# Optimization experiments

Measured on AMD Instinct MI355X. Metric: run time of the kernel, lower is better.

Reference implementation:

```python
import jax, jax.numpy as jnp
import numpy as np

LEAKY_SLOPE = 0.05        # self.alpha is overwritten to 0.05 in __init__
NEG_INF = -9.0e15         # masking constant from the source
THRESH = 0.5              # connection_threshold

B, N, F = 8, 2048, 128


def setup_inputs() -> dict:
    key = jax.random.key(0)
    k1, k2, k3, k4, k5 = jax.random.split(key, 5)
    h = jax.random.normal(k1, (B, N, F), dtype=jnp.float32)
    W = jax.random.normal(k2, (F, F), dtype=jnp.float32) * (1.414 / np.sqrt(F))
    a = jax.random.normal(k3, (2 * F, 1), dtype=jnp.float32) * 0.1
    A1 = jax.random.normal(k4, (4 * N, N), dtype=jnp.float32) * (1.414 / np.sqrt(N))
    A2 = jax.random.normal(k5, (N, 4 * N), dtype=jnp.float32) * (1.414 / np.sqrt(4 * N))
    return {"h": h, "W": W, "a": a, "A1": A1, "A2": A2}


def reference(h, W, a, A1, A2):
    f = W.shape[0]
    # Wh = h @ W^T  (torch Linear stores weight as [out, in])
    Wh = jnp.einsum('bnf,gf->bng', h, W)                       # [B,N,F]
    # additive GAT scores: e[b,i,j] = leaky_relu(Wh_i.a1 + Wh_j.a2)
    Wh1 = Wh @ a[:f, :]                                        # [B,N,1]
    Wh2 = Wh @ a[f:, :]                                        # [B,N,1]
    e = Wh1 + jnp.swapaxes(Wh2, 1, 2)                          # [B,N,N]
    e = jnp.where(e > 0, e, LEAKY_SLOPE * e)                   # LeakyReLU(0.05)
    # learned adjacency gate over last dim (computed in the original forward
    # but never used for the returned output -> dead code; kept for fidelity)
    hid = jax.nn.sigmoid(jnp.einsum('bij,hj->bih', e, A1))     # [B,N,4N]
    adj = jax.nn.sigmoid(e + jnp.einsum('bih,jh->bij', hid, A2))
    adj = jnp.where(adj > THRESH, adj, 0.0)                    # unused downstream
    # masked softmax attention over e itself
    attention = jax.nn.softmax(jnp.where(e > 0, e, NEG_INF), axis=2)
    # dropout is identity in eval mode (training=False)
    h_prime = jnp.einsum('bij,bjf->bif', attention, Wh)        # [B,N,F]
    return jax.nn.elu(h_prime)                                 # concat=True branch
```

## Files before the change

### kernel.cpp

```cpp
#include <hip/hip_runtime.h>
#include <math.h>

#define BB 8
#define NN 2048
#define FF 128
#define CH 128
#define CHSZ 16

__global__ __launch_bounds__(512) void k1_wh(
        const float* __restrict__ h, const float* __restrict__ W,
        const float* __restrict__ a, float* __restrict__ Wh,
        float* __restrict__ s1, float* __restrict__ s2) {
    __shared__ __align__(16) float Wt[64][132];
    __shared__ float hs[64][65];
    const int tid = threadIdx.x;
    const int row0 = blockIdx.x * 64;
    const int gq = tid & 15;
    const int rq = tid >> 4;

    float acc[2][8];
#pragma unroll
    for (int r = 0; r < 2; ++r)
#pragma unroll
        for (int g = 0; g < 8; ++g) acc[r][g] = 0.f;

    for (int half = 0; half < 2; ++half) {
        __syncthreads();
        for (int idx = tid; idx < 64 * 128; idx += 512) {
            int g = idx >> 6, fl = idx & 63;
            Wt[fl][g] = W[g * 128 + half * 64 + fl];
        }
        for (int idx = tid; idx < 64 * 64; idx += 512) {
            int r = idx >> 6, fl = idx & 63;
            hs[r][fl] = h[(row0 + r) * 128 + half * 64 + fl];
        }
        __syncthreads();
        for (int fl = 0; fl < 64; ++fl) {
            float4 w0 = *(const float4*)&Wt[fl][gq * 8];
            float4 w1 = *(const float4*)&Wt[fl][gq * 8 + 4];
            float h0 = hs[rq * 2 + 0][fl];
            float h1 = hs[rq * 2 + 1][fl];
            acc[0][0] += h0 * w0.x; acc[0][1] += h0 * w0.y;
            acc[0][2] += h0 * w0.z; acc[0][3] += h0 * w0.w;
            acc[0][4] += h0 * w1.x; acc[0][5] += h0 * w1.y;
            acc[0][6] += h0 * w1.z; acc[0][7] += h0 * w1.w;
            acc[1][0] += h1 * w0.x; acc[1][1] += h1 * w0.y;
            acc[1][2] += h1 * w0.z; acc[1][3] += h1 * w0.w;
            acc[1][4] += h1 * w1.x; acc[1][5] += h1 * w1.y;
            acc[1][6] += h1 * w1.z; acc[1][7] += h1 * w1.w;
        }
    }

    float a1v[8], a2v[8];
#pragma unroll
    for (int g = 0; g < 8; ++g) {
        a1v[g] = a[gq * 8 + g];
        a2v[g] = a[128 + gq * 8 + g];
    }
#pragma unroll
    for (int r = 0; r < 2; ++r) {
        int row = row0 + rq * 2 + r;
        *(float4*)&Wh[row * 128 + gq * 8] =
            make_float4(acc[r][0], acc[r][1], acc[r][2], acc[r][3]);
        *(float4*)&Wh[row * 128 + gq * 8 + 4] =
            make_float4(acc[r][4], acc[r][5], acc[r][6], acc[r][7]);
        float p1 = 0.f, p2 = 0.f;
#pragma unroll
        for (int g = 0; g < 8; ++g) {
            p1 += acc[r][g] * a1v[g];
            p2 += acc[r][g] * a2v[g];
        }
#pragma unroll
        for (int s = 1; s < 16; s <<= 1) {
            p1 += __shfl_xor(p1, s, 64);
            p2 += __shfl_xor(p2, s, 64);
        }
        if (gq == 0) { s1[row] = p1; s2[row] = p2; }
    }
}

__global__ __launch_bounds__(256) void k2_rank(
        const float* __restrict__ s2, const float* __restrict__ s1,
        int* __restrict__ idxs, float* __restrict__ ps,
        int* __restrict__ lo_arr) {
    __shared__ __align__(16) float ls[NN];
    __shared__ int part[4][64];
    __shared__ int lpart[4][64];
    __shared__ float wmax[4];
    const int t = threadIdx.x;
    const int blk = blockIdx.x;
    const int b = blk >> 5;
    const int seg = blk & 31;
    const int base = b * NN;
    float4* ls4 = (float4*)ls;
    const float4* g4 = (const float4*)(s2 + base);
    float m = -INFINITY;
    for (int i = t; i < NN / 4; i += 256) {
        float4 v4 = g4[i];
        ls4[i] = v4;
        m = fmaxf(m, fmaxf(fmaxf(v4.x, v4.y), fmaxf(v4.z, v4.w)));
    }
#pragma unroll
    for (int s = 1; s < 64; s <<= 1) m = fmaxf(m, __shfl_xor(m, s, 64));
    if ((t & 63) == 0) wmax[t >> 6] = m;
    __syncthreads();
    const float M = fmaxf(fmaxf(wmax[0], wmax[1]), fmaxf(wmax[2], wmax[3]));
    const int jj = t & 63;
    const int w  = t >> 6;
    const int j  = seg * 64 + jj;
    const float v = ls[j];
    const float s1v = s1[base + j];
    int rank = 0, cnt = 0;
#pragma unroll 8
    for (int q = 0; q < 128; ++q) {
        float4 kv = ls4[w * 128 + q];
        int kg = w * 512 + q * 4;
        rank += (kv.x < v) | ((kv.x == v) & (kg + 0 < j));
        rank += (kv.y < v) | ((kv.y == v) & (kg + 1 < j));
        rank += (kv.z < v) | ((kv.z == v) & (kg + 2 < j));
        rank += (kv.w < v) | ((kv.w == v) & (kg + 3 < j));
        cnt += (s1v + kv.x <= 0.f);
        cnt += (s1v + kv.y <= 0.f);
        cnt += (s1v + kv.z <= 0.f);
        cnt += (s1v + kv.w <= 0.f);
    }
    part[w][jj] = rank;
    lpart[w][jj] = cnt;
    __syncthreads();
    if (t < 64) {
        int r = part[0][t] + part[1][t] + part[2][t] + part[3][t];
        int jg = seg * 64 + t;
        float vv = ls[jg];
        idxs[base + r] = jg;
        ps[base + r] = expf(vv - M);
        lo_arr[base + jg] = lpart[0][t] + lpart[1][t] + lpart[2][t] + lpart[3][t];
    }
}

__global__ __launch_bounds__(128) void k3_scan(
        const float* __restrict__ Wh, const int* __restrict__ idxs,
        const float* __restrict__ ps,
        float* __restrict__ partial, float* __restrict__ psuf,
        float* __restrict__ chunktot, float* __restrict__ chunku,
        float* __restrict__ chunkp) {
    const int blk = blockIdx.x;
    const int b = blk >> 7, c = blk & 127;
    const int base = b * NN;
    const int f = threadIdx.x;
    float acc = 0.f, accu = 0.f, pacc = 0.f;
#pragma unroll
    for (int tt = CHSZ - 1; tt >= 0; --tt) {
        int r = c * CHSZ + tt;
        int jj = idxs[base + r];
        float pv = ps[base + r];
        float w = Wh[(base + jj) * 128 + f];
        acc += pv * w;
        accu += w;
        pacc += pv;
        partial[(base + r) * 128 + f] = acc;
        if (f == 0) psuf[base + r] = pacc;
    }
    chunktot[(b * CH + c) * 128 + f] = acc;
    chunku[(b * CH + c) * 128 + f] = accu;
    if (f == 0) chunkp[b * CH + c] = pacc;
}

__global__ __launch_bounds__(128) void k3b_chunksuf(
        const float* __restrict__ chunktot, const float* __restrict__ chunku,
        const float* __restrict__ chunkp,
        float* __restrict__ chunksuf, float* __restrict__ chunkpsuf,
        float* __restrict__ meanv) {
    __shared__ float lt[CH][128];
    __shared__ float lp[CH];
    const int b = blockIdx.x;
    const int f = threadIdx.x;
    float tu = 0.f;
#pragma unroll 4
    for (int c = 0; c < CH; ++c) {
        lt[c][f] = chunktot[(b * CH + c) * 128 + f];
        tu += chunku[(b * CH + c) * 128 + f];
    }
    lp[f] = chunkp[b * CH + f];
    __syncthreads();
#pragma unroll
    for (int s = 1; s < CH; s <<= 1) {
        float add = (f + s < CH) ? lp[f + s] : 0.f;
        __syncthreads();
        lp[f] += add;
        __syncthreads();
    }
    chunkpsuf[b * CH + f] = (f < CH - 1) ? lp[f + 1] : 0.f;
    float acc = 0.f;
#pragma unroll 4
    for (int c = CH - 1; c >= 0; --c) {
        chunksuf[(b * CH + c) * 128 + f] = acc;
        acc += lt[c][f];
    }
    meanv[b * 128 + f] = tu * (1.f / (float)NN);
}

__global__ __launch_bounds__(256) void k4_out(
        const int* __restrict__ lo_arr, const float* __restrict__ psuf,
        const float* __restrict__ chunkpsuf, const float* __restrict__ partial,
        const float* __restrict__ chunksuf, const float* __restrict__ meanv,
        float* __restrict__ out) {
    const int tid = threadIdx.x;
    const int rowg = blockIdx.x * 8 + (tid >> 5);
    const int fq = (tid & 31) * 4;
    const int b = rowg >> 11;
    const int base = b * NN;
    const int lo = lo_arr[rowg];
    float4 v;
    if (lo == NN) {
        v = *(const float4*)&meanv[b * 128 + fq];
    } else {
        const int c = lo >> 4;
        float4 pp = *(const float4*)&partial[(base + lo) * 128 + fq];
        float4 cs = *(const float4*)&chunksuf[(b * CH + c) * 128 + fq];
        float den = psuf[base + lo] + chunkpsuf[b * CH + c];
        v.x = (pp.x + cs.x) / den;
        v.y = (pp.y + cs.y) / den;
        v.z = (pp.z + cs.z) / den;
        v.w = (pp.w + cs.w) / den;
    }
    v.x = (v.x > 0.f) ? v.x : expm1f(v.x);
    v.y = (v.y > 0.f) ? v.y : expm1f(v.y);
    v.z = (v.z > 0.f) ? v.z : expm1f(v.z);
    v.w = (v.w > 0.f) ? v.w : expm1f(v.w);
    *(float4*)&out[rowg * 128 + fq] = v;
}

extern "C" void kernel_launch(void* const* d_in, const int* in_sizes, int n_in,
                              void* d_out, int out_size, void* d_ws, size_t ws_size,
                              hipStream_t stream) {
    (void)in_sizes; (void)n_in; (void)out_size; (void)ws_size;
    const float* h = (const float*)d_in[0];
    const float* W = (const float*)d_in[1];
    const float* a = (const float*)d_in[2];
    float* out = (float*)d_out;

    float* Wh       = (float*)d_ws;
    float* partial  = Wh + 2097152;
    float* s1       = partial + 2097152;
    float* s2       = s1 + 16384;
    float* ps       = s2 + 16384;
    float* psuf     = ps + 16384;
    int*   idxs     = (int*)(psuf + 16384);
    int*   lo_arr   = idxs + 16384;
    float* chunktot = (float*)(lo_arr + 16384);
    float* chunku   = chunktot + 131072;
    float* chunksuf = chunku + 131072;
    float* chunkp   = chunksuf + 131072;
    float* chunkpsuf= chunkp + 1024;
    float* meanv    = chunkpsuf + 1024;

    k1_wh<<<BB * NN / 64, 512, 0, stream>>>(h, W, a, Wh, s1, s2);
    k2_rank<<<BB * 32, 256, 0, stream>>>(s2, s1, idxs, ps, lo_arr);
    k3_scan<<<BB * CH, 128, 0, stream>>>(Wh, idxs, ps, partial, psuf,
                                         chunktot, chunku, chunkp);
    k3b_chunksuf<<<BB, 128, 0, stream>>>(chunktot, chunku, chunkp,
                                         chunksuf, chunkpsuf, meanv);
    k4_out<<<BB * NN / 8, 256, 0, stream>>>(lo_arr, psuf, chunkpsuf,
                                            partial, chunksuf, meanv, out);
}
```

Before: 195.2 us.

## Fuse all five stages into one cooperative persistent kernel with grid syncs

Merges the Wh projection, ranking, chunk scan, chunk suffix and output stages into a single cooperative kernel of 256 blocks. Grid-wide syncs replace the kernel launch boundaries, and a shared-memory union is reused across the phases. The aim is to remove four launch gaps and their tail effects, since each stage is short. In exchange, several stages change their block decomposition (for example the k3b suffix now uses 256 blocks instead of 8). The grid syncs carry their own cost, and the old multi-kernel path is kept as a fallback for when a cooperative launch is unsupported or fails.

```diff
diff --git a/kernel.cpp b/kernel.cpp
--- a/kernel.cpp
+++ b/kernel.cpp
@@ -1,11 +1,264 @@
 #include <hip/hip_runtime.h>
+#include <hip/hip_cooperative_groups.h>
 #include <math.h>
+
+namespace cg = cooperative_groups;
 
 #define BB 8
 #define NN 2048
 #define FF 128
 #define CH 128
 #define CHSZ 16
+
+
+struct Params {
+    const float* __restrict__ h;
+    const float* __restrict__ W;
+    const float* __restrict__ a;
+    float* __restrict__ Wh;
+    float* __restrict__ partial;
+    float* __restrict__ s1;
+    float* __restrict__ s2;
+    float* __restrict__ ps;
+    float* __restrict__ psuf;
+    int*   __restrict__ idxs;
+    int*   __restrict__ lo_arr;
+    float* __restrict__ chunktot;
+    float* __restrict__ chunku;
+    float* __restrict__ chunksuf;
+    float* __restrict__ chunkp;
+    float* __restrict__ chunkpsuf;
+    float* __restrict__ meanv;
+    float* __restrict__ out;
+};
+
+union __align__(16) SMem {
+    struct { float Wt[64][132]; float hs[64][65]; } p1;
+    struct { float ls[NN]; int part[8][64]; int lpart[8][64]; float wmax[8]; } p2;
+    struct { float lt[4][132]; float lu[4][132]; float lp[CH]; } p3b;
+};
+
+__global__ __launch_bounds__(512) void fused(Params P) {
+    __shared__ SMem sm;
+    const int tid = threadIdx.x;
+    const int blk = blockIdx.x;
+    cg::grid_group grid = cg::this_grid();
+
+    {
+        const int row0 = blk * 64;
+        const int gq = tid & 15;
+        const int rq = tid >> 4;
+
+        float acc[2][8];
+#pragma unroll
+        for (int r = 0; r < 2; ++r)
+#pragma unroll
+            for (int g = 0; g < 8; ++g) acc[r][g] = 0.f;
+
+        for (int half = 0; half < 2; ++half) {
+            __syncthreads();
+            for (int idx = tid; idx < 64 * 128; idx += 512) {
+                int g = idx >> 6, fl = idx & 63;
+                sm.p1.Wt[fl][g] = P.W[g * 128 + half * 64 + fl];
+            }
+            for (int idx = tid; idx < 64 * 64; idx += 512) {
+                int r = idx >> 6, fl = idx & 63;
+                sm.p1.hs[r][fl] = P.h[(row0 + r) * 128 + half * 64 + fl];
+            }
+            __syncthreads();
+            for (int fl = 0; fl < 64; ++fl) {
+                float4 w0 = *(const float4*)&sm.p1.Wt[fl][gq * 8];
+                float4 w1 = *(const float4*)&sm.p1.Wt[fl][gq * 8 + 4];
+                float h0 = sm.p1.hs[rq * 2 + 0][fl];
+                float h1 = sm.p1.hs[rq * 2 + 1][fl];
+                acc[0][0] += h0 * w0.x; acc[0][1] += h0 * w0.y;
+                acc[0][2] += h0 * w0.z; acc[0][3] += h0 * w0.w;
+                acc[0][4] += h0 * w1.x; acc[0][5] += h0 * w1.y;
+                acc[0][6] += h0 * w1.z; acc[0][7] += h0 * w1.w;
+                acc[1][0] += h1 * w0.x; acc[1][1] += h1 * w0.y;
+                acc[1][2] += h1 * w0.z; acc[1][3] += h1 * w0.w;
+                acc[1][4] += h1 * w1.x; acc[1][5] += h1 * w1.y;
+                acc[1][6] += h1 * w1.z; acc[1][7] += h1 * w1.w;
+            }
+        }
+
+        float a1v[8], a2v[8];
+#pragma unroll
+        for (int g = 0; g < 8; ++g) {
+            a1v[g] = P.a[gq * 8 + g];
+            a2v[g] = P.a[128 + gq * 8 + g];
+        }
+#pragma unroll
+        for (int r = 0; r < 2; ++r) {
+            int row = row0 + rq * 2 + r;
+            *(float4*)&P.Wh[row * 128 + gq * 8] =
+                make_float4(acc[r][0], acc[r][1], acc[r][2], acc[r][3]);
+            *(float4*)&P.Wh[row * 128 + gq * 8 + 4] =
+                make_float4(acc[r][4], acc[r][5], acc[r][6], acc[r][7]);
+            float p1 = 0.f, p2 = 0.f;
+#pragma unroll
+            for (int g = 0; g < 8; ++g) {
+                p1 += acc[r][g] * a1v[g];
+                p2 += acc[r][g] * a2v[g];
+            }
+#pragma unroll
+            for (int s = 1; s < 16; s <<= 1) {
+                p1 += __shfl_xor(p1, s, 64);
+                p2 += __shfl_xor(p2, s, 64);
+            }
+            if (gq == 0) { P.s1[row] = p1; P.s2[row] = p2; }
+        }
+    }
+    __threadfence();
+    grid.sync();
+
+    {
+        const int b = blk >> 5;
+        const int seg = blk & 31;
+        const int base = b * NN;
+        float* ls = sm.p2.ls;
+        float4* ls4 = (float4*)ls;
+        const float4* g4 = (const float4*)(P.s2 + base);
+        float m = -INFINITY;
+        {
+            float4 v4 = g4[tid];
+            ls4[tid] = v4;
+            m = fmaxf(fmaxf(v4.x, v4.y), fmaxf(v4.z, v4.w));
+        }
+#pragma unroll
+        for (int s = 1; s < 64; s <<= 1) m = fmaxf(m, __shfl_xor(m, s, 64));
+        if ((tid & 63) == 0) sm.p2.wmax[tid >> 6] = m;
+        __syncthreads();
+        float M = sm.p2.wmax[0];
+#pragma unroll
+        for (int i = 1; i < 8; ++i) M = fmaxf(M, sm.p2.wmax[i]);
+        const int jj = tid & 63;
+        const int w  = tid >> 6;
+        const int j  = seg * 64 + jj;
+        const float v = ls[j];
+        const float s1v = P.s1[base + j];
+        int rank = 0, cnt = 0;
+#pragma unroll 8
+        for (int q = 0; q < 64; ++q) {
+            float4 kv = ls4[w * 64 + q];
+            int kg = w * 256 + q * 4;
+            rank += (kv.x < v) | ((kv.x == v) & (kg + 0 < j));
+            rank += (kv.y < v) | ((kv.y == v) & (kg + 1 < j));
+            rank += (kv.z < v) | ((kv.z == v) & (kg + 2 < j));
+            rank += (kv.w < v) | ((kv.w == v) & (kg + 3 < j));
+            cnt += (s1v + kv.x <= 0.f);
+            cnt += (s1v + kv.y <= 0.f);
+            cnt += (s1v + kv.z <= 0.f);
+            cnt += (s1v + kv.w <= 0.f);
+        }
+        sm.p2.part[w][jj] = rank;
+        sm.p2.lpart[w][jj] = cnt;
+        __syncthreads();
+        if (tid < 64) {
+            int r = 0, lo = 0;
+#pragma unroll
+            for (int ww = 0; ww < 8; ++ww) {
+                r  += sm.p2.part[ww][tid];
+                lo += sm.p2.lpart[ww][tid];
+            }
+            int jg = seg * 64 + tid;
+            float vv = ls[jg];
+            P.idxs[base + r] = jg;
+            P.ps[base + r] = expf(vv - M);
+            P.lo_arr[base + jg] = lo;
+        }
+    }
+    __threadfence();
+    grid.sync();
+
+    {
+        const int cq = tid >> 7;
+        const int f  = tid & 127;
+        const int cg_ = blk * 4 + cq;
+        const int b = cg_ >> 7;
+        const int c = cg_ & 127;
+        const int base = b * NN;
+        float acc = 0.f, accu = 0.f, pacc = 0.f;
+#pragma unroll
+        for (int tt = CHSZ - 1; tt >= 0; --tt) {
+            int r = c * CHSZ + tt;
+            int jj2 = P.idxs[base + r];
+            float pv = P.ps[base + r];
+            float wv = P.Wh[(base + jj2) * 128 + f];
+            acc += pv * wv;
+            accu += wv;
+            pacc += pv;
+            P.partial[(base + r) * 128 + f] = acc;
+            if (f == 0) P.psuf[base + r] = pacc;
+        }
+        P.chunktot[(b * CH + c) * 128 + f] = acc;
+        P.chunku[(b * CH + c) * 128 + f] = accu;
+        if (f == 0) P.chunkp[b * CH + c] = pacc;
+    }
+    __threadfence();
+    grid.sync();
+
+    {
+        const int b  = blk >> 5;
+        const int fg = blk & 31;
+        const int c  = tid >> 2;
+        const int fl = tid & 3;
+        const int f  = fg * 4 + fl;
+        sm.p3b.lt[fl][c] = P.chunktot[(b * CH + c) * 128 + f];
+        sm.p3b.lu[fl][c] = P.chunku[(b * CH + c) * 128 + f];
+        if (tid < CH) sm.p3b.lp[tid] = P.chunkp[b * CH + tid];
+        __syncthreads();
+#pragma unroll
+        for (int s = 1; s < CH; s <<= 1) {
+            float av = 0.f, au = 0.f, ap = 0.f;
+            if (c + s < CH) { av = sm.p3b.lt[fl][c + s]; au = sm.p3b.lu[fl][c + s]; }
+            if (tid < CH && tid + s < CH) ap = sm.p3b.lp[tid + s];
+            __syncthreads();
+            sm.p3b.lt[fl][c] += av;
+            sm.p3b.lu[fl][c] += au;
+            if (tid < CH) sm.p3b.lp[tid] += ap;
+            __syncthreads();
+        }
+        P.chunksuf[(b * CH + c) * 128 + f] =
+            (c < CH - 1) ? sm.p3b.lt[fl][c + 1] : 0.f;
+        if (fg == 0 && fl == 0)
+            P.chunkpsuf[b * CH + c] = (c < CH - 1) ? sm.p3b.lp[c + 1] : 0.f;
+        if (c == 0)
+            P.meanv[b * 128 + f] = sm.p3b.lu[fl][0] * (1.f / (float)NN);
+    }
+    __threadfence();
+    grid.sync();
+
+    {
+#pragma unroll
+        for (int pass = 0; pass < 4; ++pass) {
+            const int rowg = blk * 64 + pass * 16 + (tid >> 5);
+            const int fq = (tid & 31) * 4;
+            const int b = rowg >> 11;
+            const int base = b * NN;
+            const int lo = P.lo_arr[rowg];
+            float4 v;
+            if (lo == NN) {
+                v = *(const float4*)&P.meanv[b * 128 + fq];
+            } else {
+                const int c = lo >> 4;
+                float4 pp = *(const float4*)&P.partial[(base + lo) * 128 + fq];
+                float4 cs = *(const float4*)&P.chunksuf[(b * CH + c) * 128 + fq];
+                float den = P.psuf[base + lo] + P.chunkpsuf[b * CH + c];
+                v.x = (pp.x + cs.x) / den;
+                v.y = (pp.y + cs.y) / den;
+                v.z = (pp.z + cs.z) / den;
+                v.w = (pp.w + cs.w) / den;
+            }
+            v.x = (v.x > 0.f) ? v.x : expm1f(v.x);
+            v.y = (v.y > 0.f) ? v.y : expm1f(v.y);
+            v.z = (v.z > 0.f) ? v.z : expm1f(v.z);
+            v.w = (v.w > 0.f) ? v.w : expm1f(v.w);
+            *(float4*)&P.out[rowg * 128 + fq] = v;
+        }
+    }
+}
+
 
 __global__ __launch_bounds__(512) void k1_wh(
         const float* __restrict__ h, const float* __restrict__ W,
@@ -254,12 +507,42 @@
     float* chunkpsuf= chunkp + 1024;
     float* meanv    = chunkpsuf + 1024;
 
-    k1_wh<<<BB * NN / 64, 512, 0, stream>>>(h, W, a, Wh, s1, s2);
-    k2_rank<<<BB * 32, 256, 0, stream>>>(s2, s1, idxs, ps, lo_arr);
-    k3_scan<<<BB * CH, 128, 0, stream>>>(Wh, idxs, ps, partial, psuf,
-                                         chunktot, chunku, chunkp);
-    k3b_chunksuf<<<BB, 128, 0, stream>>>(chunktot, chunku, chunkp,
-                                         chunksuf, chunkpsuf, meanv);
-    k4_out<<<BB * NN / 8, 256, 0, stream>>>(lo_arr, psuf, chunkpsuf,
-                                            partial, chunksuf, meanv, out);
-}
+    static int coop_support = -1;
+    if (coop_support < 0) {
+        int dev = 0, v = 0;
+        (void)hipGetDevice(&dev);
+        if (hipDeviceGetAttribute(&v, hipDeviceAttributeCooperativeLaunch, dev)
+                != hipSuccess) v = 0;
+        coop_support = v;
+    }
+
+    bool launched = false;
+    if (coop_support) {
+        Params P;
+        P.h = h; P.W = W; P.a = a;
+        P.Wh = Wh; P.partial = partial; P.s1 = s1; P.s2 = s2;
+        P.ps = ps; P.psuf = psuf; P.idxs = idxs; P.lo_arr = lo_arr;
+        P.chunktot = chunktot; P.chunku = chunku; P.chunksuf = chunksuf;
+        P.chunkp = chunkp; P.chunkpsuf = chunkpsuf; P.meanv = meanv;
+        P.out = out;
+        void* args[] = { (void*)&P };
+        hipError_t err = hipLaunchCooperativeKernel(
+            (const void*)fused, dim3(256), dim3(512), args, 0, stream);
+        if (err == hipSuccess) {
+            launched = true;
+        } else {
+            (void)hipGetLastError();
+        }
+    }
+
+    if (!launched) {
+        k1_wh<<<BB * NN / 64, 512, 0, stream>>>(h, W, a, Wh, s1, s2);
+        k2_rank<<<BB * 32, 256, 0, stream>>>(s2, s1, idxs, ps, lo_arr);
+        k3_scan<<<BB * CH, 128, 0, stream>>>(Wh, idxs, ps, partial, psuf,
+                                             chunktot, chunku, chunkp);
+        k3b_chunksuf<<<BB, 128, 0, stream>>>(chunktot, chunku, chunkp,
+                                             chunksuf, chunkpsuf, meanv);
+        k4_out<<<BB * NN / 8, 256, 0, stream>>>(lo_arr, psuf, chunkpsuf,
+                                                partial, chunksuf, meanv, out);
+    }
+}
```

Measured after the change: 502.2 us. 157% more time.

## Fuse chunk suffix scan into output kernel and widen rank kernel to 512 threads

Applied to the files above, without the earlier changes.

The serial single-block-per-batch chunk-suffix kernel is merged into the output kernel. Each of 256 blocks redundantly loads its batch's chunk totals into shared memory and computes the suffix sums with a parallel Hillis-Steele scan, then writes 64 output rows. This removes one launch and the low-parallelism 8-block kernel, but every block repeats the scan over 64 KB of chunk data. Separately, the rank kernel uses 512 threads so each wave compares against half as many keys.

```diff
diff --git a/kernel.cpp b/kernel.cpp
--- a/kernel.cpp
+++ b/kernel.cpp
@@ -79,14 +79,14 @@
     }
 }
 
-__global__ __launch_bounds__(256) void k2_rank(
+__global__ __launch_bounds__(512) void k2_rank(
         const float* __restrict__ s2, const float* __restrict__ s1,
         int* __restrict__ idxs, float* __restrict__ ps,
         int* __restrict__ lo_arr) {
     __shared__ __align__(16) float ls[NN];
-    __shared__ int part[4][64];
-    __shared__ int lpart[4][64];
-    __shared__ float wmax[4];
+    __shared__ int part[8][64];
+    __shared__ int lpart[8][64];
+    __shared__ float wmax[8];
     const int t = threadIdx.x;
     const int blk = blockIdx.x;
     const int b = blk >> 5;
@@ -94,17 +94,19 @@
     const int base = b * NN;
     float4* ls4 = (float4*)ls;
     const float4* g4 = (const float4*)(s2 + base);
-    float m = -INFINITY;
-    for (int i = t; i < NN / 4; i += 256) {
-        float4 v4 = g4[i];
-        ls4[i] = v4;
-        m = fmaxf(m, fmaxf(fmaxf(v4.x, v4.y), fmaxf(v4.z, v4.w)));
+    float m;
+    {
+        float4 v4 = g4[t];
+        ls4[t] = v4;
+        m = fmaxf(fmaxf(v4.x, v4.y), fmaxf(v4.z, v4.w));
     }
 #pragma unroll
     for (int s = 1; s < 64; s <<= 1) m = fmaxf(m, __shfl_xor(m, s, 64));
     if ((t & 63) == 0) wmax[t >> 6] = m;
     __syncthreads();
-    const float M = fmaxf(fmaxf(wmax[0], wmax[1]), fmaxf(wmax[2], wmax[3]));
+    float M = wmax[0];
+#pragma unroll
+    for (int i = 1; i < 8; ++i) M = fmaxf(M, wmax[i]);
     const int jj = t & 63;
     const int w  = t >> 6;
     const int j  = seg * 64 + jj;
@@ -112,9 +114,9 @@
     const float s1v = s1[base + j];
     int rank = 0, cnt = 0;
 #pragma unroll 8
-    for (int q = 0; q < 128; ++q) {
-        float4 kv = ls4[w * 128 + q];
-        int kg = w * 512 + q * 4;
+    for (int q = 0; q < 64; ++q) {
+        float4 kv = ls4[w * 64 + q];
+        int kg = w * 256 + q * 4;
         rank += (kv.x < v) | ((kv.x == v) & (kg + 0 < j));
         rank += (kv.y < v) | ((kv.y == v) & (kg + 1 < j));
         rank += (kv.z < v) | ((kv.z == v) & (kg + 2 < j));
@@ -128,12 +130,17 @@
     lpart[w][jj] = cnt;
     __syncthreads();
     if (t < 64) {
-        int r = part[0][t] + part[1][t] + part[2][t] + part[3][t];
+        int r = 0, lo = 0;
+#pragma unroll
+        for (int ww = 0; ww < 8; ++ww) {
+            r  += part[ww][t];
+            lo += lpart[ww][t];
+        }
         int jg = seg * 64 + t;
         float vv = ls[jg];
         idxs[base + r] = jg;
         ps[base + r] = expf(vv - M);
-        lo_arr[base + jg] = lpart[0][t] + lpart[1][t] + lpart[2][t] + lpart[3][t];
+        lo_arr[base + jg] = lo;
     }
 }
 
@@ -165,69 +172,88 @@
     if (f == 0) chunkp[b * CH + c] = pacc;
 }
 
-__global__ __launch_bounds__(128) void k3b_chunksuf(
+__global__ __launch_bounds__(512) void k4_merged(
         const float* __restrict__ chunktot, const float* __restrict__ chunku,
         const float* __restrict__ chunkp,
-        float* __restrict__ chunksuf, float* __restrict__ chunkpsuf,
-        float* __restrict__ meanv) {
-    __shared__ float lt[CH][128];
+        const int* __restrict__ lo_arr, const float* __restrict__ psuf,
+        const float* __restrict__ partial, float* __restrict__ out) {
+    __shared__ __align__(16) float cs[CH][132];
+    __shared__ __align__(16) float mvp[4][132];
+    __shared__ __align__(16) float mv[128];
     __shared__ float lp[CH];
-    const int b = blockIdx.x;
-    const int f = threadIdx.x;
-    float tu = 0.f;
+    const int tid = threadIdx.x;
+    const int blk = blockIdx.x;
+    const int b = blk >> 5;
+    const int base = b * NN;
+
+    {
+        const int f  = tid & 127;
+        const int r0 = tid >> 7;
+        float su = 0.f;
 #pragma unroll 4
-    for (int c = 0; c < CH; ++c) {
-        lt[c][f] = chunktot[(b * CH + c) * 128 + f];
-        tu += chunku[(b * CH + c) * 128 + f];
-    }
-    lp[f] = chunkp[b * CH + f];
+        for (int i = 0; i < 32; ++i) {
+            int c = r0 + i * 4;
+            cs[c][f] = chunktot[(b * CH + c) * 128 + f];
+            su += chunku[(b * CH + c) * 128 + f];
+        }
+        mvp[r0][f] = su;
+        if (tid < CH) lp[tid] = chunkp[b * CH + tid];
+    }
     __syncthreads();
-#pragma unroll
+    if (tid < 128)
+        mv[tid] = (mvp[0][tid] + mvp[1][tid] + mvp[2][tid] + mvp[3][tid])
+                  * (1.f / (float)NN);
+
     for (int s = 1; s < CH; s <<= 1) {
-        float add = (f + s < CH) ? lp[f + s] : 0.f;
-        __syncthreads();
-        lp[f] += add;
-        __syncthreads();
-    }
-    chunkpsuf[b * CH + f] = (f < CH - 1) ? lp[f + 1] : 0.f;
-    float acc = 0.f;
-#pragma unroll 4
-    for (int c = CH - 1; c >= 0; --c) {
-        chunksuf[(b * CH + c) * 128 + f] = acc;
-        acc += lt[c][f];
-    }
-    meanv[b * 128 + f] = tu * (1.f / (float)NN);
-}
-
-__global__ __launch_bounds__(256) void k4_out(
-        const int* __restrict__ lo_arr, const float* __restrict__ psuf,
-        const float* __restrict__ chunkpsuf, const float* __restrict__ partial,
-        const float* __restrict__ chunksuf, const float* __restrict__ meanv,
-        float* __restrict__ out) {
-    const int tid = threadIdx.x;
-    const int rowg = blockIdx.x * 8 + (tid >> 5);
-    const int fq = (tid & 31) * 4;
-    const int b = rowg >> 11;
-    const int base = b * NN;
-    const int lo = lo_arr[rowg];
-    float4 v;
-    if (lo == NN) {
-        v = *(const float4*)&meanv[b * 128 + fq];
-    } else {
-        const int c = lo >> 4;
-        float4 pp = *(const float4*)&partial[(base + lo) * 128 + fq];
-        float4 cs = *(const float4*)&chunksuf[(b * CH + c) * 128 + fq];
-        float den = psuf[base + lo] + chunkpsuf[b * CH + c];
-        v.x = (pp.x + cs.x) / den;
-        v.y = (pp.y + cs.y) / den;
-        v.z = (pp.z + cs.z) / den;
-        v.w = (pp.w + cs.w) / den;
-    }
-    v.x = (v.x > 0.f) ? v.x : expm1f(v.x);
-    v.y = (v.y > 0.f) ? v.y : expm1f(v.y);
-    v.z = (v.z > 0.f) ? v.z : expm1f(v.z);
-    v.w = (v.w > 0.f) ? v.w : expm1f(v.w);
-    *(float4*)&out[rowg * 128 + fq] = v;
+        float tmp[32];
+#pragma unroll
+        for (int i = 0; i < 32; ++i) {
+            int c = (tid >> 7) + i * 4;
+            int f = tid & 127;
+            tmp[i] = (c + s < CH) ? cs[c + s][f] : 0.f;
+        }
+        float ap = 0.f;
+        if (tid < CH && tid + s < CH) ap = lp[tid + s];
+        __syncthreads();
+#pragma unroll
+        for (int i = 0; i < 32; ++i) {
+            int c = (tid >> 7) + i * 4;
+            int f = tid & 127;
+            cs[c][f] += tmp[i];
+        }
+        if (tid < CH) lp[tid] += ap;
+        __syncthreads();
+    }
+
+#pragma unroll
+    for (int pass = 0; pass < 4; ++pass) {
+        const int rowg = blk * 64 + pass * 16 + (tid >> 5);
+        const int fq = (tid & 31) * 4;
+        const int lo = lo_arr[rowg];
+        float4 v;
+        if (lo == NN) {
+            v = make_float4(mv[fq], mv[fq + 1], mv[fq + 2], mv[fq + 3]);
+        } else {
+            const int c = lo >> 4;
+            float4 pp = *(const float4*)&partial[(base + lo) * 128 + fq];
+            float4 csv = make_float4(0.f, 0.f, 0.f, 0.f);
+            float lps = 0.f;
+            if (c < CH - 1) {
+                csv = *(const float4*)&cs[c + 1][fq];
+                lps = lp[c + 1];
+            }
+            float den = psuf[base + lo] + lps;
+            v.x = (pp.x + csv.x) / den;
+            v.y = (pp.y + csv.y) / den;
+            v.z = (pp.z + csv.z) / den;
+            v.w = (pp.w + csv.w) / den;
+        }
+        v.x = (v.x > 0.f) ? v.x : expm1f(v.x);
+        v.y = (v.y > 0.f) ? v.y : expm1f(v.y);
+        v.z = (v.z > 0.f) ? v.z : expm1f(v.z);
+        v.w = (v.w > 0.f) ? v.w : expm1f(v.w);
+        *(float4*)&out[rowg * 128 + fq] = v;
+    }
 }
 
 extern "C" void kernel_launch(void* const* d_in, const int* in_sizes, int n_in,
@@ -249,17 +275,12 @@
     int*   lo_arr   = idxs + 16384;
     float* chunktot = (float*)(lo_arr + 16384);
     float* chunku   = chunktot + 131072;
-    float* chunksuf = chunku + 131072;
-    float* chunkp   = chunksuf + 131072;
-    float* chunkpsuf= chunkp + 1024;
-    float* meanv    = chunkpsuf + 1024;
+    float* chunkp   = chunku + 131072;
 
     k1_wh<<<BB * NN / 64, 512, 0, stream>>>(h, W, a, Wh, s1, s2);
-    k2_rank<<<BB * 32, 256, 0, stream>>>(s2, s1, idxs, ps, lo_arr);
+    k2_rank<<<BB * 32, 512, 0, stream>>>(s2, s1, idxs, ps, lo_arr);
     k3_scan<<<BB * CH, 128, 0, stream>>>(Wh, idxs, ps, partial, psuf,
                                          chunktot, chunku, chunkp);
-    k3b_chunksuf<<<BB, 128, 0, stream>>>(chunktot, chunku, chunkp,
-                                         chunksuf, chunkpsuf, meanv);
-    k4_out<<<BB * NN / 8, 256, 0, stream>>>(lo_arr, psuf, chunkpsuf,
-                                            partial, chunksuf, meanv, out);
-}
+    k4_merged<<<BB * 32, 512, 0, stream>>>(chunktot, chunku, chunkp,
+                                           lo_arr, psuf, partial, out);
+}
```

Result: faster. 188.2 us (-3.6%).
